# Kernel optimization log

Measured on AMD Instinct MI355X. Metric: run time of the kernel, lower is better.

Reference implementation:

```python
import jax, jax.numpy as jnp
import numpy as np
import math

EMBED_DIM = 1024
MEMORY_DIM = 1024
MEMORY_SIZE = 2048
B, S = 8, 4096


def bitnet_linear(x, W, b):
    """Eval-mode BitNetLinear: 1.58-bit weight quant + 8-bit activation quant."""
    w_scale = jnp.mean(jnp.abs(W))
    qW = jnp.sign(W) * (jnp.abs(W) > 0.5 * w_scale).astype(W.dtype)
    i_scale = jnp.max(jnp.abs(x)) / 127.0
    qx = jnp.clip(jnp.round(x / i_scale), -128.0, 127.0)
    out = jnp.einsum('bsi,oi->bso', qx, qW) * (w_scale * i_scale)
    return out + b


def setup_inputs() -> dict:
    key = jax.random.key(0)
    ks = jax.random.split(key, 9)
    return {
        'x': jax.random.normal(ks[0], (B, S, EMBED_DIM), jnp.float32),
        'memory_keys': jax.random.normal(ks[1], (MEMORY_SIZE, MEMORY_DIM), jnp.float32),
        'memory_values': jax.random.normal(ks[2], (MEMORY_SIZE, EMBED_DIM), jnp.float32),
        'Wk': jax.random.normal(ks[3], (MEMORY_DIM, EMBED_DIM), jnp.float32) * 0.1,
        'bk': jnp.zeros((MEMORY_DIM,), jnp.float32),
        'Wv': jax.random.normal(ks[4], (EMBED_DIM, EMBED_DIM), jnp.float32) * 0.1,
        'bv': jnp.zeros((EMBED_DIM,), jnp.float32),
        'Wo': jax.random.normal(ks[5], (EMBED_DIM, EMBED_DIM), jnp.float32) * 0.1,
        'bo': jnp.zeros((EMBED_DIM,), jnp.float32),
    }


def reference(x, memory_keys, memory_values, Wk, bk, Wv, bv, Wo, bo):
    # quantized key/value projections
    query_keys = bitnet_linear(x, Wk, bk)          # [B, S, Dm]
    _query_values = bitnet_linear(x, Wv, bv)       # computed in original (used only by update path)
    # memory cross-attention over fixed bank
    similarities = jnp.einsum('bsd,md->bsm', query_keys, memory_keys)  # [B, S, M]
    attention_weights = jax.nn.softmax(similarities / math.sqrt(MEMORY_DIM), axis=-1)
    retrieved = jnp.einsum('bsm,me->bse', attention_weights, memory_values)  # [B, S, E]
    output = bitnet_linear(x + retrieved, Wo, bo)
    return output
```

## Files before the change

kernel.cpp:

```cpp
#include <hip/hip_runtime.h>
#include <hip/hip_bf16.h>
#include <stdint.h>
#include <type_traits>

typedef __attribute__((ext_vector_type(8))) short bf16x8;
typedef __attribute__((ext_vector_type(4))) float f32x4;
typedef __attribute__((ext_vector_type(4))) int i32x4;

struct Scalars {
  double sum_wk;
  double sum_wo;
  unsigned int max_x_bits;
  unsigned int max_y_bits;
};

__device__ __forceinline__ unsigned short f2bf(float f) {
  __hip_bfloat16 h = __float2bfloat16(f);
  return *reinterpret_cast<unsigned short*>(&h);
}

__device__ __forceinline__ void async16(void* lds, const void* g) {
  __builtin_amdgcn_global_load_lds((__attribute__((address_space(1))) void*)g,
                                   (__attribute__((address_space(3))) void*)lds, 16, 0, 0);
}

__device__ __forceinline__ void tile_swizzle(int nxShift, int& bx, int& by) {
  const int per = gridDim.x >> 3;
  const int tile = (blockIdx.x & 7) * per + (blockIdx.x >> 3);
  bx = tile & ((1 << nxShift) - 1);
  by = tile >> nxShift;
}

__device__ __forceinline__ f32x4 mm(bf16x8 a, bf16x8 b, f32x4 c) {
  return __builtin_amdgcn_mfma_f32_16x16x32_bf16(a, b, c, 0, 0, 0);
}
__device__ __forceinline__ i32x4 mm(i32x4 a, i32x4 b, i32x4 c) {
  return __builtin_amdgcn_mfma_i32_16x16x64_i8(a, b, c, 0, 0, 0);
}

__global__ __launch_bounds__(256) void stats_kernel(const float* __restrict__ Wk,
                                                    const float* __restrict__ Wo,
                                                    const float* __restrict__ x,
                                                    Scalars* __restrict__ sc) {
  const int which = blockIdx.y;
  size_t tid = (size_t)blockIdx.x * 256 + threadIdx.x;
  size_t stride = (size_t)gridDim.x * 256;
  if (which < 2) {
    const float* w = which ? Wo : Wk;
    const size_t n = 1048576;
    double s = 0.0;
    for (size_t i = tid * 4; i < n; i += stride * 4) {
      float4 v = *(const float4*)(w + i);
      s += (double)fabsf(v.x) + (double)fabsf(v.y) + (double)fabsf(v.z) + (double)fabsf(v.w);
    }
#pragma unroll
    for (int o = 32; o > 0; o >>= 1) s += __shfl_xor(s, o);
    __shared__ double sm[4];
    if ((threadIdx.x & 63) == 0) sm[threadIdx.x >> 6] = s;
    __syncthreads();
    if (threadIdx.x == 0)
      atomicAdd(which ? &sc->sum_wo : &sc->sum_wk, sm[0] + sm[1] + sm[2] + sm[3]);
  } else {
    const size_t n = (size_t)32768 * 1024;
    float m = 0.0f;
    for (size_t i = tid * 4; i < n; i += stride * 4) {
      float4 v = *(const float4*)(x + i);
      m = fmaxf(m, fmaxf(fmaxf(fabsf(v.x), fabsf(v.y)), fmaxf(fabsf(v.z), fabsf(v.w))));
    }
#pragma unroll
    for (int o = 32; o > 0; o >>= 1) m = fmaxf(m, __shfl_xor(m, o));
    __shared__ float smf[4];
    if ((threadIdx.x & 63) == 0) smf[threadIdx.x >> 6] = m;
    __syncthreads();
    if (threadIdx.x == 0)
      atomicMax(&sc->max_x_bits,
                __float_as_uint(fmaxf(fmaxf(smf[0], smf[1]), fmaxf(smf[2], smf[3]))));
  }
}

__global__ __launch_bounds__(256) void prep_kernel(
    const float* __restrict__ Wk, const float* __restrict__ Wo,
    const float* __restrict__ mk, const float* __restrict__ mv,
    const float* __restrict__ x, char* __restrict__ qWk8, char* __restrict__ qWo8,
    __hip_bfloat16* __restrict__ mkb, __hip_bfloat16* __restrict__ mvT,
    char* __restrict__ qx8, const Scalars* __restrict__ sc) {
  __shared__ float tl[32][33];
  const int which = blockIdx.y;
  const int t = threadIdx.x;
  size_t tid = (size_t)blockIdx.x * 256 + t;
  size_t stride = (size_t)gridDim.x * 256;
  if (which < 2) {
    const float* W = which ? Wo : Wk;
    char* q = which ? qWo8 : qWk8;
    const double sum = which ? sc->sum_wo : sc->sum_wk;
    const float thr = 0.5f * (float)(sum * (1.0 / 1048576.0));
    const size_t n = 1048576;
    for (size_t i = tid * 4; i < n; i += stride * 4) {
      float4 v = *(const float4*)(W + i);
      char4 o;
      o.x = (char)(fabsf(v.x) > thr ? (v.x > 0.f ? 1 : -1) : 0);
      o.y = (char)(fabsf(v.y) > thr ? (v.y > 0.f ? 1 : -1) : 0);
      o.z = (char)(fabsf(v.z) > thr ? (v.z > 0.f ? 1 : -1) : 0);
      o.w = (char)(fabsf(v.w) > thr ? (v.w > 0.f ? 1 : -1) : 0);
      *(char4*)(q + i) = o;
    }
  } else if (which == 2) {
    const size_t n = (size_t)2048 * 1024;
    for (size_t i = tid * 4; i < n; i += stride * 4) {
      float4 v = *(const float4*)(mk + i);
      ushort4 o;
      o.x = f2bf(v.x); o.y = f2bf(v.y); o.z = f2bf(v.z); o.w = f2bf(v.w);
      *(ushort4*)((unsigned short*)mkb + i) = o;
    }
  } else if (which == 3) {
    const int ti = blockIdx.x & 31;
    const int tj = blockIdx.x >> 5;
    const int tx = t & 31, ty = t >> 5;
#pragma unroll
    for (int r = 0; r < 4; ++r)
      tl[ty + r * 8][tx] = mv[(size_t)(tj * 32 + ty + r * 8) * 1024 + ti * 32 + tx];
    __syncthreads();
#pragma unroll
    for (int r = 0; r < 4; ++r)
      mvT[(size_t)(ti * 32 + ty + r * 8) * 2048 + tj * 32 + tx] =
          __float2bfloat16(tl[tx][ty + r * 8]);
  } else {
    const float isc = __uint_as_float(sc->max_x_bits) / 127.0f;
    const size_t n = (size_t)32768 * 1024;
    for (size_t i = tid * 4; i < n; i += stride * 4) {
      float4 v = *(const float4*)(x + i);
      char4 o;
      o.x = (char)(int)fminf(fmaxf(rintf(v.x / isc), -128.f), 127.f);
      o.y = (char)(int)fminf(fmaxf(rintf(v.y / isc), -128.f), 127.f);
      o.z = (char)(int)fminf(fmaxf(rintf(v.z / isc), -128.f), 127.f);
      o.w = (char)(int)fminf(fmaxf(rintf(v.w / isc), -128.f), 127.f);
      *(char4*)(qx8 + i) = o;
    }
  }
}

__global__ __launch_bounds__(256) void quant_act_i8_kernel(const float* __restrict__ x,
                                                           char* __restrict__ q,
                                                           const unsigned int* __restrict__ maxbits,
                                                           size_t n) {
  const float isc = __uint_as_float(*maxbits) / 127.0f;
  size_t tid = (size_t)blockIdx.x * blockDim.x + threadIdx.x;
  size_t stride = (size_t)gridDim.x * blockDim.x;
  for (size_t i = tid * 4; i < n; i += stride * 4) {
    float4 v = *(const float4*)(x + i);
    char4 o;
    o.x = (char)(int)fminf(fmaxf(rintf(v.x / isc), -128.f), 127.f);
    o.y = (char)(int)fminf(fmaxf(rintf(v.y / isc), -128.f), 127.f);
    o.z = (char)(int)fminf(fmaxf(rintf(v.z / isc), -128.f), 127.f);
    o.w = (char)(int)fminf(fmaxf(rintf(v.w / isc), -128.f), 127.f);
    *(char4*)(q + i) = o;
  }
}

__global__ __launch_bounds__(256) void softmax_kernel(__hip_bfloat16* __restrict__ sims) {
  unsigned short* row = (unsigned short*)(sims + (size_t)blockIdx.x * 2048);
  const int t = threadIdx.x;
  const int l = t & 63, wv = t >> 6;
  uint4 r4 = *(const uint4*)(row + t * 8);
  float v[8];
  v[0] = __uint_as_float(r4.x << 16); v[1] = __uint_as_float(r4.x & 0xffff0000u);
  v[2] = __uint_as_float(r4.y << 16); v[3] = __uint_as_float(r4.y & 0xffff0000u);
  v[4] = __uint_as_float(r4.z << 16); v[5] = __uint_as_float(r4.z & 0xffff0000u);
  v[6] = __uint_as_float(r4.w << 16); v[7] = __uint_as_float(r4.w & 0xffff0000u);
  float m = v[0];
#pragma unroll
  for (int i = 1; i < 8; ++i) m = fmaxf(m, v[i]);
#pragma unroll
  for (int o = 32; o > 0; o >>= 1) m = fmaxf(m, __shfl_xor(m, o));
  __shared__ float red[4], red2[4];
  if (l == 0) red[wv] = m;
  __syncthreads();
  m = fmaxf(fmaxf(red[0], red[1]), fmaxf(red[2], red[3]));
  float s = 0.f;
#pragma unroll
  for (int i = 0; i < 8; ++i) { v[i] = expf(v[i] - m); s += v[i]; }
#pragma unroll
  for (int o = 32; o > 0; o >>= 1) s += __shfl_xor(s, o);
  if (l == 0) red2[wv] = s;
  __syncthreads();
  s = red2[0] + red2[1] + red2[2] + red2[3];
  unsigned short b[8];
#pragma unroll
  for (int i = 0; i < 8; ++i) b[i] = f2bf(v[i] / s);
  uint4 o4;
  o4.x = (unsigned)b[0] | ((unsigned)b[1] << 16);
  o4.y = (unsigned)b[2] | ((unsigned)b[3] << 16);
  o4.z = (unsigned)b[4] | ((unsigned)b[5] << 16);
  o4.w = (unsigned)b[6] | ((unsigned)b[7] << 16);
  *(uint4*)(row + t * 8) = o4;
}

#define CFENCE() asm volatile("" ::: "memory")
#define BAR8() { CFENCE(); __builtin_amdgcn_s_barrier(); CFENCE(); }
#define WVM(N) asm volatile("s_waitcnt vmcnt(" #N ")" ::: "memory")

template <int EPI>
__global__ __launch_bounds__(512, 2) void gemm8(
    const char* __restrict__ A, const char* __restrict__ B, void* __restrict__ C,
    const float* __restrict__ aux, Scalars* __restrict__ sc,
    int Ndim, int KB, int nxShift) {
  constexpr bool I8 = (EPI >= 3);
  using FR  = typename std::conditional<I8, i32x4, bf16x8>::type;
  using ACC = typename std::conditional<I8, i32x4, f32x4>::type;
  __shared__ __align__(16) char lds[4][2][16384];

  int bx, by;
  tile_swizzle(nxShift, bx, by);
  const int rowBlk = by * 256, colBlk = bx * 256;

  const int t = threadIdx.x, w = t >> 6, l = t & 63;
  const int wm = w >> 2, wn = w & 3;
  const int quad = l >> 4, m16 = l & 15;
  const int NT = KB >> 7, NIT = NT >> 1;

  int voA[2][2], voB[2][2];
#pragma unroll
  for (int hf = 0; hf < 2; ++hf)
#pragma unroll
    for (int j = 0; j < 2; ++j) {
      const int idx = j * 64 + (t >> 3);
      const int kby = ((t & 7) ^ (idx & 7)) << 4;
      voA[hf][j] = (rowBlk + ((idx >> 6) << 7) + (hf << 6) + (idx & 63)) * KB + kby;
      voB[hf][j] = (colBlk + ((idx >> 5) << 6) + (hf << 5) + (idx & 31)) * KB + kby;
    }

  const char* baA[2];
  const char* baB[2];
#pragma unroll
  for (int ks = 0; ks < 2; ++ks) {
    const int x16 = ((ks << 6) + (quad << 4)) ^ ((m16 & 7) << 4);
    baA[ks] = &lds[0][0][(wm * 64 + m16) * 128 + x16];
    baB[ks] = &lds[2][0][(wn * 32 + m16) * 128 + x16];
  }

#define STG_A(slot, hf, tk)                                                         \
  if ((tk) < NT) {                                                                  \
    _Pragma("unroll") for (int j = 0; j < 2; ++j)                                   \
      async16(&lds[hf][slot][j * 8192 + (w << 10)],                                 \
              A + (((size_t)(tk)) << 7) + voA[hf][j]);                              \
  }
#define STG_B(slot, hf, tk)                                                         \
  if ((tk) < NT) {                                                                  \
    _Pragma("unroll") for (int j = 0; j < 2; ++j)                                   \
      async16(&lds[2 + (hf)][slot][j * 8192 + (w << 10)],                           \
              B + (((size_t)(tk)) << 7) + voB[hf][j]);                              \
  }

#define LD_A(dst, slot, hf, f, ks) \
  dst = *(const FR*)(baA[ks] + ((hf)*32768 + (slot)*16384 + (f)*2048));
#define LD_B(dst, slot, hf, gg, ks) \
  dst = *(const FR*)(baB[ks] + ((hf)*32768 + (slot)*16384 + (gg)*2048));

#define R_A0(s) { _Pragma("unroll") for (int f_ = 0; f_ < 4; ++f_) { LD_A(af[f_][0], s, 0, f_, 0); LD_A(af[f_][1], s, 0, f_, 1); } }
#define R_A1(s) { _Pragma("unroll") for (int f_ = 0; f_ < 4; ++f_) { LD_A(af[f_][0], s, 1, f_, 0); LD_A(af[f_][1], s, 1, f_, 1); } }
#define R_B0(s) { _Pragma("unroll") for (int g_ = 0; g_ < 2; ++g_) { LD_B(b0[g_][0], s, 0, g_, 0); LD_B(b0[g_][1], s, 0, g_, 1); } }
#define R_B1(s) { _Pragma("unroll") for (int g_ = 0; g_ < 2; ++g_) { LD_B(b1[g_][0], s, 1, g_, 0); LD_B(b1[g_][1], s, 1, g_, 1); } }

#define MM8(FO, GO, BR)                                                             \
  __builtin_amdgcn_s_setprio(1);                                                    \
  _Pragma("unroll") for (int f_ = 0; f_ < 4; ++f_)                                  \
    _Pragma("unroll") for (int g_ = 0; g_ < 2; ++g_) {                              \
      acc[(FO) + f_][(GO) + g_] = mm(af[f_][0], BR[g_][0], acc[(FO) + f_][(GO) + g_]); \
      acc[(FO) + f_][(GO) + g_] = mm(af[f_][1], BR[g_][1], acc[(FO) + f_][(GO) + g_]); \
    }                                                                               \
  __builtin_amdgcn_s_setprio(0);

#define TSTEP(s, tk, last)                                                          \
  {                                                                                 \
                                         \
    R_B1(s);                                                                        \
    STG_A((s) ^ 1, 1, (tk) + 1);                                                    \
    BAR8();                                                                         \
    MM8(0, 0, b0);                                                                  \
    BAR8();                                                                         \
        \
    STG_A(s, 0, (tk) + 2);                                                          \
    BAR8();                                                                         \
    MM8(0, 2, b1);                                                                  \
    R_A1(s);                                                                        \
    BAR8();                                                                         \
                                                                \
    STG_B(s, 0, (tk) + 2);                                                          \
    BAR8();                                                                         \
    MM8(4, 0, b0);                                                                  \
    BAR8();                                                                         \
           \
    STG_B(s, 1, (tk) + 2);                                                          \
    if (last) { WVM(0); } else { WVM(6); }                                          \
    BAR8();                                                                         \
    MM8(4, 2, b1);                                                                  \
    R_A0((s) ^ 1);                                                                  \
    R_B0((s) ^ 1);                                                                  \
  }

  FR af[4][2], b0[2][2], b1[2][2];
  ACC acc[8][4] = {};

  STG_A(0, 0, 0); STG_B(0, 0, 0); STG_B(0, 1, 0); STG_A(0, 1, 0);
  CFENCE();
  STG_A(1, 0, 1); STG_B(1, 0, 1); STG_B(1, 1, 1);
  WVM(6);
  BAR8();
  R_A0(0); R_B0(0);

  for (int it = 0; it < NIT; ++it) {
    const bool last = (it == NIT - 1);
    TSTEP(0, it * 2, last);
    TSTEP(1, it * 2 + 1, last);
  }

  float sK = 0.0f;
  if constexpr (EPI == 3)
    sK = (float)(sc->sum_wk * (1.0 / 1048576.0)) * (__uint_as_float(sc->max_x_bits) / 127.0f);
  if constexpr (EPI == 4)
    sK = (float)(sc->sum_wo * (1.0 / 1048576.0)) * (__uint_as_float(sc->max_y_bits) / 127.0f);

  float amax = 0.0f;
#pragma unroll
  for (int f = 0; f < 8; ++f) {
#pragma unroll
    for (int g = 0; g < 4; ++g) {
      const int col = colBlk + wn * 64 + g * 16 + m16;
#pragma unroll
      for (int rg = 0; rg < 4; ++rg) {
        const int row = rowBlk + wm * 128 + f * 16 + quad * 4 + rg;
        if constexpr (EPI == 1) {
          ((__hip_bfloat16*)C)[(size_t)row * Ndim + col] =
              __float2bfloat16(acc[f][g][rg] * 0.03125f);
        } else if constexpr (EPI == 2) {
          float v = acc[f][g][rg] + aux[(size_t)row * Ndim + col];
          ((float*)C)[(size_t)row * Ndim + col] = v;
          amax = fmaxf(amax, fabsf(v));
        } else if constexpr (EPI == 3) {
          ((__hip_bfloat16*)C)[(size_t)row * Ndim + col] =
              __float2bfloat16((float)acc[f][g][rg] * sK + aux[col]);
        } else {
          ((float*)C)[(size_t)row * Ndim + col] = (float)acc[f][g][rg] * sK + aux[col];
        }
      }
    }
  }

  if constexpr (EPI == 2) {
#pragma unroll
    for (int o = 32; o > 0; o >>= 1) amax = fmaxf(amax, __shfl_xor(amax, o));
    if (l == 0) atomicMax(&sc->max_y_bits, __float_as_uint(amax));
  }
#undef STG_A
#undef STG_B
#undef LD_A
#undef LD_B
#undef R_A0
#undef R_A1
#undef R_B0
#undef R_B1
#undef MM8
#undef TSTEP
}

extern "C" void kernel_launch(void* const* d_in, const int* in_sizes, int n_in,
                              void* d_out, int out_size, void* d_ws, size_t ws_size,
                              hipStream_t stream) {
  (void)in_sizes; (void)n_in; (void)out_size; (void)ws_size;
  const float* x  = (const float*)d_in[0];
  const float* mk = (const float*)d_in[1];
  const float* mv = (const float*)d_in[2];
  const float* Wk = (const float*)d_in[3];
  const float* bk = (const float*)d_in[4];
  const float* Wo = (const float*)d_in[7];
  const float* bo = (const float*)d_in[8];
  float* out = (float*)d_out;

  const int M = 32768, E = 1024, MEM = 2048;

  char* ws = (char*)d_ws;
  Scalars* sc = (Scalars*)ws;
  const size_t off0 = 256;
  char* qx8 = ws + off0;
  __hip_bfloat16* qk = (__hip_bfloat16*)(ws + off0 + (size_t)M * E);
  float* y = (float*)(ws + off0);
  const size_t off1 = off0 + (size_t)M * E * 4;
  __hip_bfloat16* sims = (__hip_bfloat16*)(ws + off1);
  char* qy8 = (char*)sims;
  const size_t off2 = off1 + (size_t)M * MEM * 2;
  char* qWk8 = ws + off2;
  char* qWo8 = qWk8 + (size_t)E * E;
  __hip_bfloat16* mkb = (__hip_bfloat16*)(qWo8 + (size_t)E * E);
  __hip_bfloat16* mvT = mkb + (size_t)MEM * E;

  hipMemsetAsync(ws, 0, 256, stream);

  stats_kernel<<<dim3(1024, 3), dim3(256), 0, stream>>>(Wk, Wo, x, sc);
  prep_kernel<<<dim3(2048, 5), dim3(256), 0, stream>>>(Wk, Wo, mk, mv, x, qWk8, qWo8,
                                                       mkb, mvT, qx8, sc);

  gemm8<3><<<dim3((E / 256) * (M / 256)), dim3(512), 0, stream>>>(
      qx8, qWk8, qk, bk, sc, E, E, 2);
  gemm8<1><<<dim3((MEM / 256) * (M / 256)), dim3(512), 0, stream>>>(
      (const char*)qk, (const char*)mkb, sims, nullptr, sc, MEM, 2 * E, 3);
  softmax_kernel<<<dim3(M), dim3(256), 0, stream>>>(sims);
  gemm8<2><<<dim3((E / 256) * (M / 256)), dim3(512), 0, stream>>>(
      (const char*)sims, (const char*)mvT, y, x, sc, E, 2 * MEM, 2);
  quant_act_i8_kernel<<<dim3(2048), dim3(256), 0, stream>>>(y, qy8, &sc->max_y_bits, (size_t)M * E);
  gemm8<4><<<dim3((E / 256) * (M / 256)), dim3(512), 0, stream>>>(
      qy8, qWo8, out, bo, sc, E, E, 2);
}
```

Baseline: 755.9 us.

## Add 256x128 bf16 GEMM for attention-value stage, wave-per-row softmax, lgkm waits

Adds a new 256x128-tile bf16 GEMM (gemm2k) with a 3-slot LDS layout to replace the 256x256 kernel for the attention-times-memory-values product. The aim is more blocks and better load balance on the long K=2048 reduction. The softmax now assigns one wavefront per row, which removes the LDS reductions and __syncthreads. Explicit lgkmcnt waits with sched barriers go into the main GEMM pipeline. Smaller tiles lower arithmetic reuse per byte loaded, and the extra waits could serialize LDS reads against the MFMAs.

```diff
diff --git a/kernel.cpp b/kernel.cpp
--- a/kernel.cpp
+++ b/kernel.cpp
@@ -158,45 +158,47 @@
 }
 
 __global__ __launch_bounds__(256) void softmax_kernel(__hip_bfloat16* __restrict__ sims) {
-  unsigned short* row = (unsigned short*)(sims + (size_t)blockIdx.x * 2048);
-  const int t = threadIdx.x;
-  const int l = t & 63, wv = t >> 6;
-  uint4 r4 = *(const uint4*)(row + t * 8);
-  float v[8];
-  v[0] = __uint_as_float(r4.x << 16); v[1] = __uint_as_float(r4.x & 0xffff0000u);
-  v[2] = __uint_as_float(r4.y << 16); v[3] = __uint_as_float(r4.y & 0xffff0000u);
-  v[4] = __uint_as_float(r4.z << 16); v[5] = __uint_as_float(r4.z & 0xffff0000u);
-  v[6] = __uint_as_float(r4.w << 16); v[7] = __uint_as_float(r4.w & 0xffff0000u);
+  const int t = threadIdx.x, l = t & 63, wv = t >> 6;
+  unsigned short* row = (unsigned short*)(sims + ((size_t)blockIdx.x * 4 + wv) * 2048);
+  uint4 r4[4];
+  float v[32];
+#pragma unroll
+  for (int c = 0; c < 4; ++c) r4[c] = *(const uint4*)(row + c * 512 + l * 8);
+#pragma unroll
+  for (int c = 0; c < 4; ++c) {
+    unsigned u0 = r4[c].x, u1 = r4[c].y, u2 = r4[c].z, u3 = r4[c].w;
+    v[c * 8 + 0] = __uint_as_float(u0 << 16); v[c * 8 + 1] = __uint_as_float(u0 & 0xffff0000u);
+    v[c * 8 + 2] = __uint_as_float(u1 << 16); v[c * 8 + 3] = __uint_as_float(u1 & 0xffff0000u);
+    v[c * 8 + 4] = __uint_as_float(u2 << 16); v[c * 8 + 5] = __uint_as_float(u2 & 0xffff0000u);
+    v[c * 8 + 6] = __uint_as_float(u3 << 16); v[c * 8 + 7] = __uint_as_float(u3 & 0xffff0000u);
+  }
   float m = v[0];
 #pragma unroll
-  for (int i = 1; i < 8; ++i) m = fmaxf(m, v[i]);
+  for (int i = 1; i < 32; ++i) m = fmaxf(m, v[i]);
 #pragma unroll
   for (int o = 32; o > 0; o >>= 1) m = fmaxf(m, __shfl_xor(m, o));
-  __shared__ float red[4], red2[4];
-  if (l == 0) red[wv] = m;
-  __syncthreads();
-  m = fmaxf(fmaxf(red[0], red[1]), fmaxf(red[2], red[3]));
   float s = 0.f;
 #pragma unroll
-  for (int i = 0; i < 8; ++i) { v[i] = expf(v[i] - m); s += v[i]; }
+  for (int i = 0; i < 32; ++i) { v[i] = expf(v[i] - m); s += v[i]; }
 #pragma unroll
   for (int o = 32; o > 0; o >>= 1) s += __shfl_xor(s, o);
-  if (l == 0) red2[wv] = s;
-  __syncthreads();
-  s = red2[0] + red2[1] + red2[2] + red2[3];
-  unsigned short b[8];
-#pragma unroll
-  for (int i = 0; i < 8; ++i) b[i] = f2bf(v[i] / s);
-  uint4 o4;
-  o4.x = (unsigned)b[0] | ((unsigned)b[1] << 16);
-  o4.y = (unsigned)b[2] | ((unsigned)b[3] << 16);
-  o4.z = (unsigned)b[4] | ((unsigned)b[5] << 16);
-  o4.w = (unsigned)b[6] | ((unsigned)b[7] << 16);
-  *(uint4*)(row + t * 8) = o4;
+#pragma unroll
+  for (int c = 0; c < 4; ++c) {
+    unsigned short b[8];
+#pragma unroll
+    for (int j = 0; j < 8; ++j) b[j] = f2bf(v[c * 8 + j] / s);
+    uint4 o4;
+    o4.x = (unsigned)b[0] | ((unsigned)b[1] << 16);
+    o4.y = (unsigned)b[2] | ((unsigned)b[3] << 16);
+    o4.z = (unsigned)b[4] | ((unsigned)b[5] << 16);
+    o4.w = (unsigned)b[6] | ((unsigned)b[7] << 16);
+    *(uint4*)(row + c * 512 + l * 8) = o4;
+  }
 }
 
 #define CFENCE() asm volatile("" ::: "memory")
 #define BAR8() { CFENCE(); __builtin_amdgcn_s_barrier(); CFENCE(); }
+#define WLGKM(N) { asm volatile("s_waitcnt lgkmcnt(" #N ")" ::: "memory"); __builtin_amdgcn_sched_barrier(0); }
 #define WVM(N) asm volatile("s_waitcnt vmcnt(" #N ")" ::: "memory")
 
 template <int EPI>
@@ -272,24 +274,20 @@
 
 #define TSTEP(s, tk, last)                                                          \
   {                                                                                 \
-                                         \
     R_B1(s);                                                                        \
     STG_A((s) ^ 1, 1, (tk) + 1);                                                    \
-    BAR8();                                                                         \
+    BAR8(); WLGKM(4);                                                               \
     MM8(0, 0, b0);                                                                  \
     BAR8();                                                                         \
-        \
     STG_A(s, 0, (tk) + 2);                                                          \
-    BAR8();                                                                         \
+    BAR8(); WLGKM(0);                                                               \
     MM8(0, 2, b1);                                                                  \
     R_A1(s);                                                                        \
     BAR8();                                                                         \
-                                                                \
     STG_B(s, 0, (tk) + 2);                                                          \
-    BAR8();                                                                         \
+    BAR8(); WLGKM(0);                                                               \
     MM8(4, 0, b0);                                                                  \
     BAR8();                                                                         \
-           \
     STG_B(s, 1, (tk) + 2);                                                          \
     if (last) { WVM(0); } else { WVM(6); }                                          \
     BAR8();                                                                         \
@@ -363,6 +361,110 @@
 #undef TSTEP
 }
 
+__global__ __launch_bounds__(512, 2) void gemm2k(
+    const char* __restrict__ A, const char* __restrict__ B, float* __restrict__ C,
+    const float* __restrict__ aux, Scalars* __restrict__ sc,
+    int Ndim, int KB, int nxShift) {
+  __shared__ __align__(16) char lds[3][2][8192];
+
+  int bx, by;
+  tile_swizzle(nxShift, bx, by);
+  const int rowBlk = by * 256, colBlk = bx * 128;
+
+  const int t = threadIdx.x, w = t >> 6, l = t & 63;
+  const int wm = w >> 2, wn = w & 3;
+  const int quad = l >> 4, m16 = l & 15;
+  const int NT = KB >> 6;
+
+  const int r = t >> 2;
+  const int cg = ((t & 3) ^ ((r >> 1) & 3)) << 4;
+  int voA[2];
+  voA[0] = (rowBlk + ((r >> 6) << 7) + (r & 63)) * KB + cg;
+  voA[1] = voA[0] + 64 * KB;
+  const int voB = (colBlk + r) * KB + cg;
+
+  const int cofs = (quad ^ ((m16 >> 1) & 3)) << 4;
+  const char* bA = &lds[0][0][0] + (wm * 64 + m16) * 64 + cofs;
+  const char* bB = &lds[2][0][0] + (wn * 32 + m16) * 64 + cofs;
+
+#define G2_STG_A(slot, hf, tk) \
+  if ((tk) < NT) async16(&lds[hf][slot][t * 16], A + (((size_t)(tk)) << 6) + voA[hf]);
+#define G2_STG_B(slot, tk) \
+  if ((tk) < NT) async16(&lds[2][slot][t * 16], B + (((size_t)(tk)) << 6) + voB);
+#define G2_LD_A(dst, slot, hf, f) \
+  dst = *(const bf16x8*)(bA + ((hf) * 16384 + (slot) * 8192 + (f) * 1024));
+#define G2_LD_B(dst, slot, g) \
+  dst = *(const bf16x8*)(bB + ((slot) * 8192 + (g) * 1024));
+
+#define G2_RA0(s) { _Pragma("unroll") for (int f_ = 0; f_ < 4; ++f_) G2_LD_A(af0[f_], s, 0, f_); }
+#define G2_RA1(s) { _Pragma("unroll") for (int f_ = 0; f_ < 4; ++f_) G2_LD_A(af1[f_], s, 1, f_); }
+#define G2_RB(s)  { _Pragma("unroll") for (int g_ = 0; g_ < 2; ++g_) G2_LD_B(b[g_], s, g_); }
+
+#define G2_MM(MH, AF)                                                               \
+  __builtin_amdgcn_s_setprio(1);                                                    \
+  _Pragma("unroll") for (int f_ = 0; f_ < 4; ++f_)                                  \
+    _Pragma("unroll") for (int g_ = 0; g_ < 2; ++g_)                                \
+      acc[(MH) * 4 + f_][g_] = mm(AF[f_], b[g_], acc[(MH) * 4 + f_][g_]);           \
+  __builtin_amdgcn_s_setprio(0);
+
+#define G2_TSTEP(s, kt, last)                                                       \
+  {                                                                                 \
+    G2_STG_A((s) ^ 1, 1, (kt) + 1);                                                 \
+    BAR8(); WLGKM(0);                                                               \
+    G2_MM(0, af0);                                                                  \
+    G2_RA1(s);                                                                      \
+    BAR8();                                                                         \
+    G2_STG_A(s, 0, (kt) + 2); G2_STG_B(s, (kt) + 2);                                \
+    if (last) { WVM(0); } else { WVM(2); }                                          \
+    BAR8(); WLGKM(0);                                                               \
+    G2_MM(1, af1);                                                                  \
+    G2_RA0((s) ^ 1); G2_RB((s) ^ 1);                                                \
+  }
+
+  bf16x8 af0[4], af1[4], b[2];
+  f32x4 acc[8][2] = {};
+
+  G2_STG_A(0, 0, 0); G2_STG_B(0, 0); G2_STG_A(0, 1, 0);
+  CFENCE();
+  G2_STG_A(1, 0, 1); G2_STG_B(1, 1);
+  WVM(2);
+  BAR8();
+  G2_RA0(0); G2_RB(0);
+
+  for (int it = 0; it < NT / 2; ++it) {
+    G2_TSTEP(0, it * 2, it * 2 >= NT - 2);
+    G2_TSTEP(1, it * 2 + 1, it * 2 + 1 >= NT - 2);
+  }
+
+  float amax = 0.0f;
+#pragma unroll
+  for (int f = 0; f < 8; ++f) {
+#pragma unroll
+    for (int g = 0; g < 2; ++g) {
+      const int col = colBlk + wn * 32 + g * 16 + m16;
+#pragma unroll
+      for (int rg = 0; rg < 4; ++rg) {
+        const int row = rowBlk + wm * 128 + f * 16 + quad * 4 + rg;
+        float v = acc[f][g][rg] + aux[(size_t)row * Ndim + col];
+        C[(size_t)row * Ndim + col] = v;
+        amax = fmaxf(amax, fabsf(v));
+      }
+    }
+  }
+#pragma unroll
+  for (int o = 32; o > 0; o >>= 1) amax = fmaxf(amax, __shfl_xor(amax, o));
+  if (l == 0) atomicMax(&sc->max_y_bits, __float_as_uint(amax));
+#undef G2_STG_A
+#undef G2_STG_B
+#undef G2_LD_A
+#undef G2_LD_B
+#undef G2_RA0
+#undef G2_RA1
+#undef G2_RB
+#undef G2_MM
+#undef G2_TSTEP
+}
+
 extern "C" void kernel_launch(void* const* d_in, const int* in_sizes, int n_in,
                               void* d_out, int out_size, void* d_ws, size_t ws_size,
                               hipStream_t stream) {
@@ -403,9 +505,9 @@
       qx8, qWk8, qk, bk, sc, E, E, 2);
   gemm8<1><<<dim3((MEM / 256) * (M / 256)), dim3(512), 0, stream>>>(
       (const char*)qk, (const char*)mkb, sims, nullptr, sc, MEM, 2 * E, 3);
-  softmax_kernel<<<dim3(M), dim3(256), 0, stream>>>(sims);
-  gemm8<2><<<dim3((E / 256) * (M / 256)), dim3(512), 0, stream>>>(
-      (const char*)sims, (const char*)mvT, y, x, sc, E, 2 * MEM, 2);
+  softmax_kernel<<<dim3(M / 4), dim3(256), 0, stream>>>(sims);
+  gemm2k<<<dim3((E / 128) * (M / 256)), dim3(512), 0, stream>>>(
+      (const char*)sims, (const char*)mvT, y, x, sc, E, 2 * MEM, 3);
   quant_act_i8_kernel<<<dim3(2048), dim3(256), 0, stream>>>(y, qy8, &sc->max_y_bits, (size_t)M * E);
   gemm8<4><<<dim3((E / 256) * (M / 256)), dim3(512), 0, stream>>>(
       qy8, qWo8, out, bo, sc, E, E, 2);
```

Measured after the change: 778.7 us. 3.0% more time.

## Store x+retrieved as bf16, use wave-per-row softmax, add LDS waitcnts in GEMM

Applied to the files above, without the earlier changes.

The intermediate y = x + retrieved is now written as bf16 instead of fp32, and the activation-quant kernel reads bf16, which halves that round trip through memory. The softmax handles one row per wavefront, with four rows per block, so the LDS reductions and __syncthreads are gone. The GEMM main loop gains explicit lgkmcnt waits plus sched_barriers before the MFMA groups. Rounding y to bf16 before int8 quantization can shift some quantized values by one step relative to fp32.

```diff
diff --git a/kernel.cpp b/kernel.cpp
--- a/kernel.cpp
+++ b/kernel.cpp
@@ -139,64 +139,74 @@
   }
 }
 
-__global__ __launch_bounds__(256) void quant_act_i8_kernel(const float* __restrict__ x,
-                                                           char* __restrict__ q,
-                                                           const unsigned int* __restrict__ maxbits,
-                                                           size_t n) {
+__global__ __launch_bounds__(256) void quant_act_bf16_kernel(
+    const __hip_bfloat16* __restrict__ y, char* __restrict__ q,
+    const unsigned int* __restrict__ maxbits, size_t n) {
   const float isc = __uint_as_float(*maxbits) / 127.0f;
   size_t tid = (size_t)blockIdx.x * blockDim.x + threadIdx.x;
   size_t stride = (size_t)gridDim.x * blockDim.x;
-  for (size_t i = tid * 4; i < n; i += stride * 4) {
-    float4 v = *(const float4*)(x + i);
-    char4 o;
-    o.x = (char)(int)fminf(fmaxf(rintf(v.x / isc), -128.f), 127.f);
-    o.y = (char)(int)fminf(fmaxf(rintf(v.y / isc), -128.f), 127.f);
-    o.z = (char)(int)fminf(fmaxf(rintf(v.z / isc), -128.f), 127.f);
-    o.w = (char)(int)fminf(fmaxf(rintf(v.w / isc), -128.f), 127.f);
-    *(char4*)(q + i) = o;
+  for (size_t i = tid * 8; i < n; i += stride * 8) {
+    uint4 r = *(const uint4*)((const unsigned short*)y + i);
+    float v[8];
+    v[0] = __uint_as_float(r.x << 16); v[1] = __uint_as_float(r.x & 0xffff0000u);
+    v[2] = __uint_as_float(r.y << 16); v[3] = __uint_as_float(r.y & 0xffff0000u);
+    v[4] = __uint_as_float(r.z << 16); v[5] = __uint_as_float(r.z & 0xffff0000u);
+    v[6] = __uint_as_float(r.w << 16); v[7] = __uint_as_float(r.w & 0xffff0000u);
+    char o[8];
+#pragma unroll
+    for (int j = 0; j < 8; ++j)
+      o[j] = (char)(int)fminf(fmaxf(rintf(v[j] / isc), -128.f), 127.f);
+    uint2 pk;
+    pk.x = (unsigned char)o[0] | ((unsigned)(unsigned char)o[1] << 8) |
+           ((unsigned)(unsigned char)o[2] << 16) | ((unsigned)(unsigned char)o[3] << 24);
+    pk.y = (unsigned char)o[4] | ((unsigned)(unsigned char)o[5] << 8) |
+           ((unsigned)(unsigned char)o[6] << 16) | ((unsigned)(unsigned char)o[7] << 24);
+    *(uint2*)(q + i) = pk;
   }
 }
 
 __global__ __launch_bounds__(256) void softmax_kernel(__hip_bfloat16* __restrict__ sims) {
-  unsigned short* row = (unsigned short*)(sims + (size_t)blockIdx.x * 2048);
-  const int t = threadIdx.x;
-  const int l = t & 63, wv = t >> 6;
-  uint4 r4 = *(const uint4*)(row + t * 8);
-  float v[8];
-  v[0] = __uint_as_float(r4.x << 16); v[1] = __uint_as_float(r4.x & 0xffff0000u);
-  v[2] = __uint_as_float(r4.y << 16); v[3] = __uint_as_float(r4.y & 0xffff0000u);
-  v[4] = __uint_as_float(r4.z << 16); v[5] = __uint_as_float(r4.z & 0xffff0000u);
-  v[6] = __uint_as_float(r4.w << 16); v[7] = __uint_as_float(r4.w & 0xffff0000u);
+  const int t = threadIdx.x, l = t & 63, wv = t >> 6;
+  unsigned short* row = (unsigned short*)(sims + ((size_t)blockIdx.x * 4 + wv) * 2048);
+  uint4 r4[4];
+  float v[32];
+#pragma unroll
+  for (int c = 0; c < 4; ++c) r4[c] = *(const uint4*)(row + c * 512 + l * 8);
+#pragma unroll
+  for (int c = 0; c < 4; ++c) {
+    unsigned u0 = r4[c].x, u1 = r4[c].y, u2 = r4[c].z, u3 = r4[c].w;
+    v[c * 8 + 0] = __uint_as_float(u0 << 16); v[c * 8 + 1] = __uint_as_float(u0 & 0xffff0000u);
+    v[c * 8 + 2] = __uint_as_float(u1 << 16); v[c * 8 + 3] = __uint_as_float(u1 & 0xffff0000u);
+    v[c * 8 + 4] = __uint_as_float(u2 << 16); v[c * 8 + 5] = __uint_as_float(u2 & 0xffff0000u);
+    v[c * 8 + 6] = __uint_as_float(u3 << 16); v[c * 8 + 7] = __uint_as_float(u3 & 0xffff0000u);
+  }
   float m = v[0];
 #pragma unroll
-  for (int i = 1; i < 8; ++i) m = fmaxf(m, v[i]);
+  for (int i = 1; i < 32; ++i) m = fmaxf(m, v[i]);
 #pragma unroll
   for (int o = 32; o > 0; o >>= 1) m = fmaxf(m, __shfl_xor(m, o));
-  __shared__ float red[4], red2[4];
-  if (l == 0) red[wv] = m;
-  __syncthreads();
-  m = fmaxf(fmaxf(red[0], red[1]), fmaxf(red[2], red[3]));
   float s = 0.f;
 #pragma unroll
-  for (int i = 0; i < 8; ++i) { v[i] = expf(v[i] - m); s += v[i]; }
+  for (int i = 0; i < 32; ++i) { v[i] = expf(v[i] - m); s += v[i]; }
 #pragma unroll
   for (int o = 32; o > 0; o >>= 1) s += __shfl_xor(s, o);
-  if (l == 0) red2[wv] = s;
-  __syncthreads();
-  s = red2[0] + red2[1] + red2[2] + red2[3];
-  unsigned short b[8];
-#pragma unroll
-  for (int i = 0; i < 8; ++i) b[i] = f2bf(v[i] / s);
-  uint4 o4;
-  o4.x = (unsigned)b[0] | ((unsigned)b[1] << 16);
-  o4.y = (unsigned)b[2] | ((unsigned)b[3] << 16);
-  o4.z = (unsigned)b[4] | ((unsigned)b[5] << 16);
-  o4.w = (unsigned)b[6] | ((unsigned)b[7] << 16);
-  *(uint4*)(row + t * 8) = o4;
+#pragma unroll
+  for (int c = 0; c < 4; ++c) {
+    unsigned short b[8];
+#pragma unroll
+    for (int j = 0; j < 8; ++j) b[j] = f2bf(v[c * 8 + j] / s);
+    uint4 o4;
+    o4.x = (unsigned)b[0] | ((unsigned)b[1] << 16);
+    o4.y = (unsigned)b[2] | ((unsigned)b[3] << 16);
+    o4.z = (unsigned)b[4] | ((unsigned)b[5] << 16);
+    o4.w = (unsigned)b[6] | ((unsigned)b[7] << 16);
+    *(uint4*)(row + c * 512 + l * 8) = o4;
+  }
 }
 
 #define CFENCE() asm volatile("" ::: "memory")
 #define BAR8() { CFENCE(); __builtin_amdgcn_s_barrier(); CFENCE(); }
+#define WLGKM(N) { asm volatile("s_waitcnt lgkmcnt(" #N ")" ::: "memory"); __builtin_amdgcn_sched_barrier(0); }
 #define WVM(N) asm volatile("s_waitcnt vmcnt(" #N ")" ::: "memory")
 
 template <int EPI>
@@ -272,24 +282,20 @@
 
 #define TSTEP(s, tk, last)                                                          \
   {                                                                                 \
-                                         \
     R_B1(s);                                                                        \
     STG_A((s) ^ 1, 1, (tk) + 1);                                                    \
-    BAR8();                                                                         \
+    BAR8(); WLGKM(4);                                                               \
     MM8(0, 0, b0);                                                                  \
     BAR8();                                                                         \
-        \
     STG_A(s, 0, (tk) + 2);                                                          \
-    BAR8();                                                                         \
+    BAR8(); WLGKM(0);                                                               \
     MM8(0, 2, b1);                                                                  \
     R_A1(s);                                                                        \
     BAR8();                                                                         \
-                                                                \
     STG_B(s, 0, (tk) + 2);                                                          \
-    BAR8();                                                                         \
+    BAR8(); WLGKM(0);                                                               \
     MM8(4, 0, b0);                                                                  \
     BAR8();                                                                         \
-           \
     STG_B(s, 1, (tk) + 2);                                                          \
     if (last) { WVM(0); } else { WVM(6); }                                          \
     BAR8();                                                                         \
@@ -334,7 +340,7 @@
               __float2bfloat16(acc[f][g][rg] * 0.03125f);
         } else if constexpr (EPI == 2) {
           float v = acc[f][g][rg] + aux[(size_t)row * Ndim + col];
-          ((float*)C)[(size_t)row * Ndim + col] = v;
+          ((__hip_bfloat16*)C)[(size_t)row * Ndim + col] = __float2bfloat16(v);
           amax = fmaxf(amax, fabsf(v));
         } else if constexpr (EPI == 3) {
           ((__hip_bfloat16*)C)[(size_t)row * Ndim + col] =
@@ -383,7 +389,7 @@
   const size_t off0 = 256;
   char* qx8 = ws + off0;
   __hip_bfloat16* qk = (__hip_bfloat16*)(ws + off0 + (size_t)M * E);
-  float* y = (float*)(ws + off0);
+  __hip_bfloat16* yb = (__hip_bfloat16*)(ws + off0);
   const size_t off1 = off0 + (size_t)M * E * 4;
   __hip_bfloat16* sims = (__hip_bfloat16*)(ws + off1);
   char* qy8 = (char*)sims;
@@ -403,10 +409,11 @@
       qx8, qWk8, qk, bk, sc, E, E, 2);
   gemm8<1><<<dim3((MEM / 256) * (M / 256)), dim3(512), 0, stream>>>(
       (const char*)qk, (const char*)mkb, sims, nullptr, sc, MEM, 2 * E, 3);
-  softmax_kernel<<<dim3(M), dim3(256), 0, stream>>>(sims);
+  softmax_kernel<<<dim3(M / 4), dim3(256), 0, stream>>>(sims);
   gemm8<2><<<dim3((E / 256) * (M / 256)), dim3(512), 0, stream>>>(
-      (const char*)sims, (const char*)mvT, y, x, sc, E, 2 * MEM, 2);
-  quant_act_i8_kernel<<<dim3(2048), dim3(256), 0, stream>>>(y, qy8, &sc->max_y_bits, (size_t)M * E);
+      (const char*)sims, (const char*)mvT, yb, x, sc, E, 2 * MEM, 2);
+  quant_act_bf16_kernel<<<dim3(2048), dim3(256), 0, stream>>>(yb, qy8, &sc->max_y_bits,
+                                                              (size_t)M * E);
   gemm8<4><<<dim3((E / 256) * (M / 256)), dim3(512), 0, stream>>>(
       qy8, qWo8, out, bo, sc, E, E, 2);
 }
```

Measured after the change: 760.9 us. Within noise of the previous version (+0.7%).
